# Kernel tuning notes

Hardware: AMD Instinct MI355X
Metric: run time of the kernel (lower is better)

The kernel has to match this reference:

```python
import jax, jax.numpy as jnp
import numpy as np

B, S, IN, H, C = 4, 1024, 1024, 256, 8

def setup_inputs() -> dict:
    key = jax.random.key(0)
    ks = jax.random.split(key, 9)
    scale_in = 1.0 / np.sqrt(IN)
    scale_h2 = 1.0 / np.sqrt(2 * H)
    return {
        "seq_feats": jax.random.normal(ks[0], (B, S, IN), dtype=jnp.float32),
        "U": jax.random.normal(ks[1], (H, C, H), dtype=jnp.float32) * 0.02,
        "W_weight": jax.random.uniform(ks[2], (C, 2 * H), minval=-scale_h2, maxval=scale_h2, dtype=jnp.float32),
        "W_bias": jax.random.uniform(ks[3], (C,), minval=-scale_h2, maxval=scale_h2, dtype=jnp.float32),
        "start_w": jax.random.uniform(ks[4], (H, IN), minval=-scale_in, maxval=scale_in, dtype=jnp.float32),
        "start_b": jax.random.uniform(ks[5], (H,), minval=-scale_in, maxval=scale_in, dtype=jnp.float32),
        "end_w": jax.random.uniform(ks[6], (H, IN), minval=-scale_in, maxval=scale_in, dtype=jnp.float32),
        "end_b": jax.random.uniform(ks[7], (H,), minval=-scale_in, maxval=scale_in, dtype=jnp.float32),
    }

def reference(seq_feats, U, W_weight, W_bias, start_w, start_b, end_w, end_b):
    # Hs, He: [b, s, h]
    Hs = jnp.einsum('bsi,hi->bsh', seq_feats, start_w) + start_b
    He = jnp.einsum('bsi,hi->bsh', seq_feats, end_w) + end_b
    # biaffine: [b, s, e, c]
    biaff = jnp.einsum('bsh,hcg,beg->bsec', Hs, U, He)
    # Linear over concat([Hs_repeat, He_repeat]) == split-weight broadcast sum
    Ws, We = W_weight[:, :256], W_weight[:, 256:]
    lin = (jnp.einsum('bsh,ch->bsc', Hs, Ws)[:, :, None, :]
           + jnp.einsum('beh,ch->bec', He, We)[:, None, :, :]
           + W_bias)
    return biaff + lin
```

## Files before the change

### kernel.cpp

```cpp
#include <hip/hip_runtime.h>
#include <stdint.h>


#define BDIM 256

typedef float f32x4 __attribute__((ext_vector_type(4)));
typedef __bf16 bf16x8 __attribute__((ext_vector_type(8)));
typedef unsigned int u32;
typedef unsigned short u16;
typedef const __attribute__((address_space(1))) u32* gas_ptr;
typedef __attribute__((address_space(3))) u32* las_ptr;

static __device__ __forceinline__ void load_lds16(const void* g, void* l) {
  __builtin_amdgcn_global_load_lds((gas_ptr)g, (las_ptr)l, 16, 0, 0);
}

static __device__ __forceinline__ u16 f32_to_bf16(float f) {
  union { float f; u32 u; } v; v.f = f;
  u32 r = v.u + 0x7FFFu + ((v.u >> 16) & 1u);
  return (u16)(r >> 16);
}
static __device__ __forceinline__ float bf16lo_to_f32(u32 u) {
  union { u32 u; float f; } v; v.u = u << 16;
  return v.f;
}
static __device__ __forceinline__ float bf16hi_to_f32(u32 u) {
  union { u32 u; float f; } v; v.u = u & 0xFFFF0000u;
  return v.f;
}

static __device__ __forceinline__ void stage32(u16* lds, int dst, const u16* src,
                                               int srow, int ld, int kcol, int tid) {
  const int r = tid >> 3;
  const int sl = tid & 7;
  load_lds16(src + (size_t)(srow + r) * ld + kcol + ((sl ^ (r & 7)) << 3),
             &lds[dst + tid * 8]);
}

static __device__ __forceinline__ bf16x8 rd64(const u16* lds, int base, int row, int kslot) {
  return *reinterpret_cast<const bf16x8*>(&lds[base + row * 64 + ((kslot ^ (row & 7)) << 3)]);
}

__global__ __launch_bounds__(BDIM, 4)
void gemm128_biaff(const u16* __restrict__ Tall,
                   const u16* __restrict__ Bg,
                   float* __restrict__ Out,
                   const float* __restrict__ linSall,
                   const float* __restrict__ linEall)
{
  __shared__ u16 lds[2 * 8192];

  const int tid  = threadIdx.x;
  const int lane = tid & 63;
  const int wv   = tid >> 6;
  const int wr   = wv >> 1;
  const int wc   = wv & 1;
  const int rA   = lane & 15;
  const int kq   = lane >> 4;
  const int z    = blockIdx.z;

  int id = blockIdx.y * gridDim.x + blockIdx.x;
  id = (id & 7) * 64 + (id >> 3);
  const int n0 = (id & 7) * 128;
  const int m0 = (id >> 3) * 128;

  const u16* Ag  = Tall + (size_t)z * (8192 * 256);
  const u16* Bgz = Bg   + (size_t)z * (1024 * 512);

  f32x4 acc[4][4];
#pragma unroll
  for (int i = 0; i < 4; ++i)
#pragma unroll
    for (int j = 0; j < 4; ++j) acc[i][j] = (f32x4)0.f;

#pragma unroll 1
  for (int kt = 0; kt < 256; kt += 64) {
#pragma unroll
    for (int h = 0; h < 4; ++h)
      stage32(lds, h * 2048, Ag, m0 + h * 32, 256, kt, tid);
#pragma unroll
    for (int h = 0; h < 4; ++h)
      stage32(lds, 8192 + h * 2048, Bgz, n0 + h * 32, 512, kt, tid);
    __syncthreads();

    bf16x8 aF[4][2], bF[4][2];
#pragma unroll
    for (int mi = 0; mi < 4; ++mi)
#pragma unroll
      for (int ks = 0; ks < 2; ++ks)
        aF[mi][ks] = rd64(lds, 0, wr * 64 + mi * 16 + rA, (ks << 2) | kq);
#pragma unroll
    for (int ni = 0; ni < 4; ++ni)
#pragma unroll
      for (int ks = 0; ks < 2; ++ks)
        bF[ni][ks] = rd64(lds, 8192, wc * 64 + ni * 16 + rA, (ks << 2) | kq);
#pragma unroll
    for (int mi = 0; mi < 4; ++mi)
#pragma unroll
      for (int ni = 0; ni < 4; ++ni)
#pragma unroll
        for (int ks = 0; ks < 2; ++ks)
          acc[mi][ni] = __builtin_amdgcn_mfma_f32_16x16x32_bf16(
              aF[mi][ks], bF[ni][ks], acc[mi][ni], 0, 0, 0);
    __syncthreads();
  }

  float* OutZ = Out + (size_t)z * 8388608;
  const float* lS = linSall + (size_t)z * 8192;
  const float* lE = linEall + (size_t)z * 8192;
#pragma unroll
  for (int mi = 0; mi < 4; ++mi) {
#pragma unroll
    for (int ni = 0; ni < 4; ++ni) {
      const int mBase = m0 + wr * 64 + mi * 16 + kq * 4;
      const int e = n0 + wc * 64 + ni * 16 + rA;
      const int s = mBase >> 3;
      const int c0 = mBase & 7;
      const float4 ls4 = *reinterpret_cast<const float4*>(lS + mBase);
      const float4 le4 = *reinterpret_cast<const float4*>(lE + (e << 3) + c0);
      float4 o;
      o.x = acc[mi][ni][0] + ls4.x + le4.x;
      o.y = acc[mi][ni][1] + ls4.y + le4.y;
      o.z = acc[mi][ni][2] + ls4.z + le4.z;
      o.w = acc[mi][ni][3] + ls4.w + le4.w;
      *reinterpret_cast<float4*>(OutZ + ((size_t)s << 13) + ((size_t)e << 3) + c0) = o;
    }
  }
}

template <int IM, int EPI>
__global__ __launch_bounds__(BDIM, 2)
void gemm_bt(const u16* __restrict__ Aall,
             const u16* __restrict__ Ball,
             void* __restrict__ OutAll,
             const int N, const int K, const int lda, const int ldb,
             const float* __restrict__ bias0,
             const float* __restrict__ bias1)
{
  constexpr int WM = IM * 16;
  constexpr int TM = 2 * WM;

  __shared__ u16 lsA[TM * 32];
  __shared__ u16 lsB[128 * 32];

  const int tid  = threadIdx.x;
  const int lane = tid & 63;
  const int wv   = tid >> 6;
  const int wr   = wv >> 1;
  const int wc   = wv & 1;

  const int gx = gridDim.x;
  const int nwg = gx * gridDim.y;
  int id = blockIdx.y * gx + blockIdx.x;
  {
    const int q = nwg >> 3;
    id = (id & 7) * q + (id >> 3);
  }
  const int n0 = (id % gx) * 128;
  const int m0 = (id / gx) * TM;

  const u16* A  = Aall;
  const u16* Bm = Ball;

  f32x4 acc[IM][4];
#pragma unroll
  for (int i = 0; i < IM; ++i)
#pragma unroll
    for (int j = 0; j < 4; ++j) acc[i][j] = (f32x4)0.f;

  const int rA = lane & 15;
  const int ko = (lane >> 4) * 8;

  for (int kt = 0; kt < K; kt += 32) {
    constexpr int CA = TM * 4;
#pragma unroll
    for (int it = 0; it < CA / BDIM; ++it) {
      const int chunk = it * BDIM + tid;
      const int row = chunk >> 2;
      const int ce = (chunk & 3) * 8;
      load_lds16(A + (size_t)(m0 + row) * lda + (kt + ce), &lsA[chunk * 8]);
    }
#pragma unroll
    for (int it = 0; it < 2; ++it) {
      const int chunk = it * BDIM + tid;
      const int row = chunk >> 2;
      const int ce = (chunk & 3) * 8;
      load_lds16(Bm + (size_t)(n0 + row) * ldb + (kt + ce), &lsB[chunk * 8]);
    }
    __syncthreads();

    bf16x8 aF[IM], bF[4];
#pragma unroll
    for (int i = 0; i < IM; ++i)
      aF[i] = *reinterpret_cast<const bf16x8*>(&lsA[(wr * WM + i * 16 + rA) * 32 + ko]);
#pragma unroll
    for (int j = 0; j < 4; ++j)
      bF[j] = *reinterpret_cast<const bf16x8*>(&lsB[(wc * 64 + j * 16 + rA) * 32 + ko]);
#pragma unroll
    for (int i = 0; i < IM; ++i)
#pragma unroll
      for (int j = 0; j < 4; ++j)
        acc[i][j] = __builtin_amdgcn_mfma_f32_16x16x32_bf16(aF[i], bF[j], acc[i][j], 0, 0, 0);
    __syncthreads();
  }

  const int rgr = (lane >> 4) * 4;
  u16* Out = (u16*)OutAll;
#pragma unroll
  for (int i = 0; i < IM; ++i) {
#pragma unroll
    for (int j = 0; j < 4; ++j) {
      const int mBase = m0 + wr * WM + i * 16 + rgr;
      const int n = n0 + wc * 64 + j * 16 + rA;
      float bn = 0.f;
      if constexpr (EPI == 1) bn = (n < 256) ? bias0[n] : bias1[n - 256];
#pragma unroll
      for (int r = 0; r < 4; ++r) {
        Out[(size_t)(mBase + r) * N + n] = f32_to_bf16(acc[i][j][r] + bn);
      }
    }
  }
}

__global__ __launch_bounds__(BDIM, 2)
void k2lin(const u16* __restrict__ Hboth,
           const u16* __restrict__ Utbf,
           u16* __restrict__ Tbf,
           const float* __restrict__ Ww,
           const float* __restrict__ Wb,
           float* __restrict__ linS,
           float* __restrict__ linE)
{
  const int bid = blockIdx.x;
  const int tid = threadIdx.x;

  if (bid >= 512) {
    const int idx = (bid - 512) * BDIM + tid;
    const int m = idx >> 3;
    const int c = idx & 7;
    const uint4* hs4 = reinterpret_cast<const uint4*>(Hboth + (size_t)m * 512);
    const uint4* he4 = reinterpret_cast<const uint4*>(Hboth + (size_t)m * 512 + 256);
    const float* wsp = Ww + c * 512;
    const float* wep = wsp + 256;
    float s1 = 0.f, s2 = 0.f;
#pragma unroll 4
    for (int t = 0; t < 32; ++t) {
      const uint4 a = hs4[t];
      const uint4 b = he4[t];
      const u32 aw[4] = {a.x, a.y, a.z, a.w};
      const u32 bw[4] = {b.x, b.y, b.z, b.w};
#pragma unroll
      for (int q = 0; q < 4; ++q) {
        const int h = t * 8 + q * 2;
        s1 += bf16lo_to_f32(aw[q]) * wsp[h] + bf16hi_to_f32(aw[q]) * wsp[h + 1];
        s2 += bf16lo_to_f32(bw[q]) * wep[h] + bf16hi_to_f32(bw[q]) * wep[h + 1];
      }
    }
    linS[idx] = s1;
    linE[idx] = s2 + Wb[c];
    return;
  }

  __shared__ u16 lsA[128 * 32];
  __shared__ u16 lsB[128 * 32];

  int id = bid;
  id = (id & 7) * 64 + (id >> 3);
  const int n0 = (id & 15) * 128;
  const int m0 = (id >> 4) * 128;

  const int lane = tid & 63;
  const int wv   = tid >> 6;
  const int wr   = wv >> 1;
  const int wc   = wv & 1;
  const int rA   = lane & 15;
  const int ko   = (lane >> 4) * 8;

  f32x4 acc[4][4];
#pragma unroll
  for (int i = 0; i < 4; ++i)
#pragma unroll
    for (int j = 0; j < 4; ++j) acc[i][j] = (f32x4)0.f;

  for (int kt = 0; kt < 256; kt += 32) {
#pragma unroll
    for (int it = 0; it < 2; ++it) {
      const int chunk = it * BDIM + tid;
      const int row = chunk >> 2;
      const int ce = (chunk & 3) * 8;
      load_lds16(Hboth + (size_t)(m0 + row) * 512 + (kt + ce), &lsA[chunk * 8]);
      load_lds16(Utbf + (size_t)(n0 + row) * 256 + (kt + ce), &lsB[chunk * 8]);
    }
    __syncthreads();

    bf16x8 aF[4], bF[4];
#pragma unroll
    for (int i = 0; i < 4; ++i)
      aF[i] = *reinterpret_cast<const bf16x8*>(&lsA[(wr * 64 + i * 16 + rA) * 32 + ko]);
#pragma unroll
    for (int j = 0; j < 4; ++j)
      bF[j] = *reinterpret_cast<const bf16x8*>(&lsB[(wc * 64 + j * 16 + rA) * 32 + ko]);
#pragma unroll
    for (int i = 0; i < 4; ++i)
#pragma unroll
      for (int j = 0; j < 4; ++j)
        acc[i][j] = __builtin_amdgcn_mfma_f32_16x16x32_bf16(aF[i], bF[j], acc[i][j], 0, 0, 0);
    __syncthreads();
  }

  const int rgr = (lane >> 4) * 4;
#pragma unroll
  for (int i = 0; i < 4; ++i) {
#pragma unroll
    for (int j = 0; j < 4; ++j) {
      const int mBase = m0 + wr * 64 + i * 16 + rgr;
      const int n = n0 + wc * 64 + j * 16 + rA;
#pragma unroll
      for (int r = 0; r < 4; ++r)
        Tbf[(size_t)(mBase + r) * 2048 + n] = f32_to_bf16(acc[i][j][r]);
    }
  }
}

__global__ void prep_kernel(const float* __restrict__ seq,
                            const float* __restrict__ sw,
                            const float* __restrict__ ew,
                            const float* __restrict__ U,
                            u16* __restrict__ Xbf,
                            u16* __restrict__ wbf,
                            u16* __restrict__ Ut)
{
  const int bid = blockIdx.x;
  const int tid = threadIdx.x;
  if (bid < 4096) {
    const int i = bid * 1024 + tid * 4;
    const float4 v = *reinterpret_cast<const float4*>(seq + i);
    ushort4 o;
    o.x = f32_to_bf16(v.x); o.y = f32_to_bf16(v.y);
    o.z = f32_to_bf16(v.z); o.w = f32_to_bf16(v.w);
    *reinterpret_cast<ushort4*>(Xbf + i) = o;
  } else if (bid < 4608) {
    const int i = (bid - 4096) * 1024 + tid * 4;
    const float* src = (i < 262144) ? (sw + i) : (ew + (i - 262144));
    const float4 v = *reinterpret_cast<const float4*>(src);
    ushort4 o;
    o.x = f32_to_bf16(v.x); o.y = f32_to_bf16(v.y);
    o.z = f32_to_bf16(v.z); o.w = f32_to_bf16(v.w);
    *reinterpret_cast<ushort4*>(wbf + i) = o;
  } else {
    const int i = (bid - 4608) * 1024 + tid * 4;
    const int n = i >> 8;
    const int h = i & 255;
    ushort4 o;
    o.x = f32_to_bf16(U[(size_t)(h + 0) * 2048 + n]);
    o.y = f32_to_bf16(U[(size_t)(h + 1) * 2048 + n]);
    o.z = f32_to_bf16(U[(size_t)(h + 2) * 2048 + n]);
    o.w = f32_to_bf16(U[(size_t)(h + 3) * 2048 + n]);
    *reinterpret_cast<ushort4*>(Ut + i) = o;
  }
}

extern "C" void kernel_launch(void* const* d_in, const int* in_sizes, int n_in,
                              void* d_out, int out_size, void* d_ws, size_t ws_size,
                              hipStream_t stream)
{
  const float* seq = (const float*)d_in[0];
  const float* U   = (const float*)d_in[1];
  const float* Ww  = (const float*)d_in[2];
  const float* Wb  = (const float*)d_in[3];
  const float* sw  = (const float*)d_in[4];
  const float* sb  = (const float*)d_in[5];
  const float* ew  = (const float*)d_in[6];
  const float* eb  = (const float*)d_in[7];
  float* out = (float*)d_out;

  u16* Xbf   = (u16*)d_ws;
  u16* wbf   = Xbf  + 4194304;
  u16* Utbf  = wbf  + 524288;
  u16* Hboth = Utbf + 524288;
  u16* Tbf   = Hboth + 2097152;
  float* linS = (float*)(Tbf + 8388608);
  float* linE = linS + 32768;

  prep_kernel<<<5120, BDIM, 0, stream>>>(seq, sw, ew, U, Xbf, wbf, Utbf);

  gemm_bt<2, 1><<<dim3(4, 64, 1), BDIM, 0, stream>>>(
      Xbf, wbf, Hboth, 512, 1024, 1024, 1024, sb, eb);

  k2lin<<<640, BDIM, 0, stream>>>(Hboth, Utbf, Tbf, Ww, Wb, linS, linE);

  gemm128_biaff<<<dim3(8, 64, 4), BDIM, 0, stream>>>(
      Tbf, Hboth + 256, out, linS, linE);
}
```

Before: 90.30 us.

## Fuse Hs·U projection into biaffine GEMM, keeping T tile in LDS

The T = Hs·U intermediate GEMM and the biaffine GEMM become one kernel. Each 512-thread block computes the T tile for 16 sequence positions straight into LDS as bf16, then loops over all 1024 end positions streaming He tiles against it. This removes the 16 MB Tbf round trip through global memory and one launch, and the linear-term kernel is split out on its own. In exchange the grid is only 256 blocks with 80 KB of dynamic LDS each, so occupancy drops. The U fragments are also read directly from global memory without staging.

```diff
diff --git a/kernel.cpp b/kernel.cpp
--- a/kernel.cpp
+++ b/kernel.cpp
@@ -29,101 +29,139 @@
   return v.f;
 }
 
-static __device__ __forceinline__ void stage32(u16* lds, int dst, const u16* src,
-                                               int srow, int ld, int kcol, int tid) {
-  const int r = tid >> 3;
-  const int sl = tid & 7;
-  load_lds16(src + (size_t)(srow + r) * ld + kcol + ((sl ^ (r & 7)) << 3),
-             &lds[dst + tid * 8]);
-}
-
 static __device__ __forceinline__ bf16x8 rd64(const u16* lds, int base, int row, int kslot) {
   return *reinterpret_cast<const bf16x8*>(&lds[base + row * 64 + ((kslot ^ (row & 7)) << 3)]);
 }
 
-__global__ __launch_bounds__(BDIM, 4)
-void gemm128_biaff(const u16* __restrict__ Tall,
-                   const u16* __restrict__ Bg,
-                   float* __restrict__ Out,
-                   const float* __restrict__ linSall,
-                   const float* __restrict__ linEall)
-{
-  __shared__ u16 lds[2 * 8192];
+__global__ __launch_bounds__(512, 2)
+void k23(const u16* __restrict__ Hboth,
+         const u16* __restrict__ Utbf,
+         float* __restrict__ Out,
+         const float* __restrict__ linSall,
+         const float* __restrict__ linEall)
+{
+  extern __shared__ u16 lds[];
 
   const int tid  = threadIdx.x;
   const int lane = tid & 63;
   const int wv   = tid >> 6;
-  const int wr   = wv >> 1;
-  const int wc   = wv & 1;
   const int rA   = lane & 15;
   const int kq   = lane >> 4;
-  const int z    = blockIdx.z;
-
-  int id = blockIdx.y * gridDim.x + blockIdx.x;
-  id = (id & 7) * 64 + (id >> 3);
-  const int n0 = (id & 7) * 128;
-  const int m0 = (id >> 3) * 128;
-
-  const u16* Ag  = Tall + (size_t)z * (8192 * 256);
-  const u16* Bgz = Bg   + (size_t)z * (1024 * 512);
-
-  f32x4 acc[4][4];
-#pragma unroll
-  for (int i = 0; i < 4; ++i)
-#pragma unroll
-    for (int j = 0; j < 4; ++j) acc[i][j] = (f32x4)0.f;
+
+  int id = (blockIdx.x & 7) * 32 + (blockIdx.x >> 3);
+  const int z  = id >> 6;
+  const int s0 = (id & 63) * 16;
+
+  const u16* HsZ = Hboth + ((size_t)(z * 1024 + s0)) * 512;
+  const u16* HeZ = Hboth + ((size_t)(z * 1024)) * 512 + 256;
+
+  bf16x8 bq[8];
+#pragma unroll
+  for (int ks = 0; ks < 8; ++ks)
+    bq[ks] = *reinterpret_cast<const bf16x8*>(HsZ + (size_t)rA * 512 + ks * 32 + kq * 8);
+
+  f32x4 p[16];
+#pragma unroll
+  for (int t = 0; t < 16; ++t) p[t] = (f32x4)0.f;
+
+  const u16* UtW = Utbf + ((size_t)(wv * 256 + rA)) * 256 + kq * 8;
+#pragma unroll
+  for (int ks = 0; ks < 8; ++ks) {
+#pragma unroll
+    for (int t = 0; t < 16; ++t) {
+      const bf16x8 a = *reinterpret_cast<const bf16x8*>(UtW + t * 16 * 256 + ks * 32);
+      p[t] = __builtin_amdgcn_mfma_f32_16x16x32_bf16(a, bq[ks], p[t], 0, 0, 0);
+    }
+  }
+
+  {
+    const int m = rA * 8 + wv;
+    const int mbase = m * 64;
+#pragma unroll
+    for (int t = 0; t < 16; ++t) {
+      ushort4 w4;
+      w4.x = f32_to_bf16(p[t][0]);
+      w4.y = f32_to_bf16(p[t][1]);
+      w4.z = f32_to_bf16(p[t][2]);
+      w4.w = f32_to_bf16(p[t][3]);
+      const int kslot = (t & 3) * 2 + (kq >> 1);
+      const int addr = (t >> 2) * 8192 + mbase + ((kslot ^ wv) << 3) + (kq & 1) * 4;
+      *reinterpret_cast<ushort4*>(&lds[addr]) = w4;
+    }
+  }
+  __syncthreads();
+
+  const int wr = wv >> 2;
+  const int wc = wv & 3;
+
+  float* OutZ = Out + (size_t)z * 8388608;
+  const float* lS = linSall + ((size_t)(z * 1024 + s0)) * 8;
+  const float* lE = linEall + (size_t)z * 8192;
+
+  float4 ls4[4];
+#pragma unroll
+  for (int mi = 0; mi < 4; ++mi)
+    ls4[mi] = *reinterpret_cast<const float4*>(lS + wr * 64 + mi * 16 + kq * 4);
 
 #pragma unroll 1
-  for (int kt = 0; kt < 256; kt += 64) {
-#pragma unroll
-    for (int h = 0; h < 4; ++h)
-      stage32(lds, h * 2048, Ag, m0 + h * 32, 256, kt, tid);
-#pragma unroll
-    for (int h = 0; h < 4; ++h)
-      stage32(lds, 8192 + h * 2048, Bgz, n0 + h * 32, 512, kt, tid);
-    __syncthreads();
-
-    bf16x8 aF[4][2], bF[4][2];
-#pragma unroll
-    for (int mi = 0; mi < 4; ++mi)
-#pragma unroll
-      for (int ks = 0; ks < 2; ++ks)
-        aF[mi][ks] = rd64(lds, 0, wr * 64 + mi * 16 + rA, (ks << 2) | kq);
-#pragma unroll
-    for (int ni = 0; ni < 4; ++ni)
-#pragma unroll
-      for (int ks = 0; ks < 2; ++ks)
-        bF[ni][ks] = rd64(lds, 8192, wc * 64 + ni * 16 + rA, (ks << 2) | kq);
-#pragma unroll
-    for (int mi = 0; mi < 4; ++mi)
-#pragma unroll
-      for (int ni = 0; ni < 4; ++ni)
+  for (int nt = 0; nt < 8; ++nt) {
+    const int e0 = nt * 128;
+    f32x4 acc[4][2];
+#pragma unroll
+    for (int i = 0; i < 4; ++i)
+#pragma unroll
+      for (int j = 0; j < 2; ++j) acc[i][j] = (f32x4)0.f;
+
+#pragma unroll 1
+    for (int kt = 0; kt < 4; ++kt) {
+#pragma unroll
+      for (int hh = 0; hh < 2; ++hh) {
+        const int idx = hh * 512 + tid;
+        const int r = idx >> 3;
+        const int sl = idx & 7;
+        load_lds16(HeZ + (size_t)(e0 + r) * 512 + kt * 64 + ((sl ^ (r & 7)) << 3),
+                   &lds[32768 + idx * 8]);
+      }
+      __syncthreads();
+
+      bf16x8 aF[4][2], bF[2][2];
+#pragma unroll
+      for (int mi = 0; mi < 4; ++mi)
 #pragma unroll
         for (int ks = 0; ks < 2; ++ks)
-          acc[mi][ni] = __builtin_amdgcn_mfma_f32_16x16x32_bf16(
-              aF[mi][ks], bF[ni][ks], acc[mi][ni], 0, 0, 0);
-    __syncthreads();
-  }
-
-  float* OutZ = Out + (size_t)z * 8388608;
-  const float* lS = linSall + (size_t)z * 8192;
-  const float* lE = linEall + (size_t)z * 8192;
-#pragma unroll
-  for (int mi = 0; mi < 4; ++mi) {
-#pragma unroll
-    for (int ni = 0; ni < 4; ++ni) {
-      const int mBase = m0 + wr * 64 + mi * 16 + kq * 4;
-      const int e = n0 + wc * 64 + ni * 16 + rA;
+          aF[mi][ks] = rd64(lds, kt * 8192, wr * 64 + mi * 16 + rA, (ks << 2) | kq);
+#pragma unroll
+      for (int ni = 0; ni < 2; ++ni)
+#pragma unroll
+        for (int ks = 0; ks < 2; ++ks)
+          bF[ni][ks] = rd64(lds, 32768, wc * 32 + ni * 16 + rA, (ks << 2) | kq);
+#pragma unroll
+      for (int mi = 0; mi < 4; ++mi)
+#pragma unroll
+        for (int ni = 0; ni < 2; ++ni)
+#pragma unroll
+          for (int ks = 0; ks < 2; ++ks)
+            acc[mi][ni] = __builtin_amdgcn_mfma_f32_16x16x32_bf16(
+                aF[mi][ks], bF[ni][ks], acc[mi][ni], 0, 0, 0);
+      __syncthreads();
+    }
+
+#pragma unroll
+    for (int mi = 0; mi < 4; ++mi) {
+      const int mBase = wr * 64 + mi * 16 + kq * 4;
       const int s = mBase >> 3;
       const int c0 = mBase & 7;
-      const float4 ls4 = *reinterpret_cast<const float4*>(lS + mBase);
-      const float4 le4 = *reinterpret_cast<const float4*>(lE + (e << 3) + c0);
-      float4 o;
-      o.x = acc[mi][ni][0] + ls4.x + le4.x;
-      o.y = acc[mi][ni][1] + ls4.y + le4.y;
-      o.z = acc[mi][ni][2] + ls4.z + le4.z;
-      o.w = acc[mi][ni][3] + ls4.w + le4.w;
-      *reinterpret_cast<float4*>(OutZ + ((size_t)s << 13) + ((size_t)e << 3) + c0) = o;
+#pragma unroll
+      for (int ni = 0; ni < 2; ++ni) {
+        const int e = e0 + wc * 32 + ni * 16 + rA;
+        const float4 le4 = *reinterpret_cast<const float4*>(lE + e * 8 + c0);
+        float4 o;
+        o.x = acc[mi][ni][0] + ls4[mi].x + le4.x;
+        o.y = acc[mi][ni][1] + ls4[mi].y + le4.y;
+        o.z = acc[mi][ni][2] + ls4[mi].z + le4.z;
+        o.w = acc[mi][ni][3] + ls4[mi].w + le4.w;
+        *reinterpret_cast<float4*>(OutZ + (((size_t)(s0 + s)) << 13) + ((size_t)e << 3) + c0) = o;
+      }
     }
   }
 }
@@ -222,104 +260,36 @@
   }
 }
 
-__global__ __launch_bounds__(BDIM, 2)
-void k2lin(const u16* __restrict__ Hboth,
-           const u16* __restrict__ Utbf,
-           u16* __restrict__ Tbf,
-           const float* __restrict__ Ww,
-           const float* __restrict__ Wb,
-           float* __restrict__ linS,
-           float* __restrict__ linE)
-{
-  const int bid = blockIdx.x;
-  const int tid = threadIdx.x;
-
-  if (bid >= 512) {
-    const int idx = (bid - 512) * BDIM + tid;
-    const int m = idx >> 3;
-    const int c = idx & 7;
-    const uint4* hs4 = reinterpret_cast<const uint4*>(Hboth + (size_t)m * 512);
-    const uint4* he4 = reinterpret_cast<const uint4*>(Hboth + (size_t)m * 512 + 256);
-    const float* wsp = Ww + c * 512;
-    const float* wep = wsp + 256;
-    float s1 = 0.f, s2 = 0.f;
+__global__ __launch_bounds__(BDIM)
+void lin_kernel(const u16* __restrict__ Hboth,
+                const float* __restrict__ Ww,
+                const float* __restrict__ Wb,
+                float* __restrict__ linS,
+                float* __restrict__ linE)
+{
+  const int idx = blockIdx.x * BDIM + threadIdx.x;
+  const int m = idx >> 3;
+  const int c = idx & 7;
+  const uint4* hs4 = reinterpret_cast<const uint4*>(Hboth + (size_t)m * 512);
+  const uint4* he4 = reinterpret_cast<const uint4*>(Hboth + (size_t)m * 512 + 256);
+  const float* wsp = Ww + c * 512;
+  const float* wep = wsp + 256;
+  float s1 = 0.f, s2 = 0.f;
 #pragma unroll 4
-    for (int t = 0; t < 32; ++t) {
-      const uint4 a = hs4[t];
-      const uint4 b = he4[t];
-      const u32 aw[4] = {a.x, a.y, a.z, a.w};
-      const u32 bw[4] = {b.x, b.y, b.z, b.w};
-#pragma unroll
-      for (int q = 0; q < 4; ++q) {
-        const int h = t * 8 + q * 2;
-        s1 += bf16lo_to_f32(aw[q]) * wsp[h] + bf16hi_to_f32(aw[q]) * wsp[h + 1];
-        s2 += bf16lo_to_f32(bw[q]) * wep[h] + bf16hi_to_f32(bw[q]) * wep[h + 1];
-      }
-    }
-    linS[idx] = s1;
-    linE[idx] = s2 + Wb[c];
-    return;
-  }
-
-  __shared__ u16 lsA[128 * 32];
-  __shared__ u16 lsB[128 * 32];
-
-  int id = bid;
-  id = (id & 7) * 64 + (id >> 3);
-  const int n0 = (id & 15) * 128;
-  const int m0 = (id >> 4) * 128;
-
-  const int lane = tid & 63;
-  const int wv   = tid >> 6;
-  const int wr   = wv >> 1;
-  const int wc   = wv & 1;
-  const int rA   = lane & 15;
-  const int ko   = (lane >> 4) * 8;
-
-  f32x4 acc[4][4];
-#pragma unroll
-  for (int i = 0; i < 4; ++i)
-#pragma unroll
-    for (int j = 0; j < 4; ++j) acc[i][j] = (f32x4)0.f;
-
-  for (int kt = 0; kt < 256; kt += 32) {
-#pragma unroll
-    for (int it = 0; it < 2; ++it) {
-      const int chunk = it * BDIM + tid;
-      const int row = chunk >> 2;
-      const int ce = (chunk & 3) * 8;
-      load_lds16(Hboth + (size_t)(m0 + row) * 512 + (kt + ce), &lsA[chunk * 8]);
-      load_lds16(Utbf + (size_t)(n0 + row) * 256 + (kt + ce), &lsB[chunk * 8]);
-    }
-    __syncthreads();
-
-    bf16x8 aF[4], bF[4];
-#pragma unroll
-    for (int i = 0; i < 4; ++i)
-      aF[i] = *reinterpret_cast<const bf16x8*>(&lsA[(wr * 64 + i * 16 + rA) * 32 + ko]);
-#pragma unroll
-    for (int j = 0; j < 4; ++j)
-      bF[j] = *reinterpret_cast<const bf16x8*>(&lsB[(wc * 64 + j * 16 + rA) * 32 + ko]);
-#pragma unroll
-    for (int i = 0; i < 4; ++i)
-#pragma unroll
-      for (int j = 0; j < 4; ++j)
-        acc[i][j] = __builtin_amdgcn_mfma_f32_16x16x32_bf16(aF[i], bF[j], acc[i][j], 0, 0, 0);
-    __syncthreads();
-  }
-
-  const int rgr = (lane >> 4) * 4;
-#pragma unroll
-  for (int i = 0; i < 4; ++i) {
-#pragma unroll
-    for (int j = 0; j < 4; ++j) {
-      const int mBase = m0 + wr * 64 + i * 16 + rgr;
-      const int n = n0 + wc * 64 + j * 16 + rA;
-#pragma unroll
-      for (int r = 0; r < 4; ++r)
-        Tbf[(size_t)(mBase + r) * 2048 + n] = f32_to_bf16(acc[i][j][r]);
-    }
-  }
+  for (int t = 0; t < 32; ++t) {
+    const uint4 a = hs4[t];
+    const uint4 b = he4[t];
+    const u32 aw[4] = {a.x, a.y, a.z, a.w};
+    const u32 bw[4] = {b.x, b.y, b.z, b.w};
+#pragma unroll
+    for (int q = 0; q < 4; ++q) {
+      const int h = t * 8 + q * 2;
+      s1 += bf16lo_to_f32(aw[q]) * wsp[h] + bf16hi_to_f32(aw[q]) * wsp[h + 1];
+      s2 += bf16lo_to_f32(bw[q]) * wep[h] + bf16hi_to_f32(bw[q]) * wep[h + 1];
+    }
+  }
+  linS[idx] = s1;
+  linE[idx] = s2 + Wb[c];
 }
 
 __global__ void prep_kernel(const float* __restrict__ seq,
@@ -378,8 +348,7 @@
   u16* wbf   = Xbf  + 4194304;
   u16* Utbf  = wbf  + 524288;
   u16* Hboth = Utbf + 524288;
-  u16* Tbf   = Hboth + 2097152;
-  float* linS = (float*)(Tbf + 8388608);
+  float* linS = (float*)(Hboth + 2097152);
   float* linE = linS + 32768;
 
   prep_kernel<<<5120, BDIM, 0, stream>>>(seq, sw, ew, U, Xbf, wbf, Utbf);
@@ -387,8 +356,9 @@
   gemm_bt<2, 1><<<dim3(4, 64, 1), BDIM, 0, stream>>>(
       Xbf, wbf, Hboth, 512, 1024, 1024, 1024, sb, eb);
 
-  k2lin<<<640, BDIM, 0, stream>>>(Hboth, Utbf, Tbf, Ww, Wb, linS, linE);
-
-  gemm128_biaff<<<dim3(8, 64, 4), BDIM, 0, stream>>>(
-      Tbf, Hboth + 256, out, linS, linE);
-}
+  lin_kernel<<<128, BDIM, 0, stream>>>(Hboth, Ww, Wb, linS, linE);
+
+  hipFuncSetAttribute(reinterpret_cast<const void*>(&k23),
+                      hipFuncAttributeMaxDynamicSharedMemorySize, 81920);
+  k23<<<256, 512, 81920, stream>>>(Hboth, Utbf, out, linS, linE);
+}
```

Measured after the change: 123.7 us. 37.0% more time.

## Replace projection GEMM with 64x64-tile swizzled-LDS kernel using K=64 steps

Applied to the files above, without the earlier changes.

Replaces the generic gemm_bt used for the Hs/He projection with a dedicated kernel that uses 64x64 output tiles, a 512-block grid, and K steps of 64 staged through an XOR-swizzled LDS layout. The smaller tiles double the block count, which should fill more CUs, and the swizzle should cut LDS bank conflicts. The cost is lower per-block data reuse and more global traffic per FLOP. The launch also allows higher occupancy via launch bounds of 4.

```diff
diff --git a/kernel.cpp b/kernel.cpp
--- a/kernel.cpp
+++ b/kernel.cpp
@@ -39,6 +39,78 @@
 
 static __device__ __forceinline__ bf16x8 rd64(const u16* lds, int base, int row, int kslot) {
   return *reinterpret_cast<const bf16x8*>(&lds[base + row * 64 + ((kslot ^ (row & 7)) << 3)]);
+}
+
+__global__ __launch_bounds__(BDIM, 4)
+void k1(const u16* __restrict__ Xbf,
+        const u16* __restrict__ wbf,
+        u16* __restrict__ Hboth,
+        const float* __restrict__ sb,
+        const float* __restrict__ eb)
+{
+  __shared__ u16 lds[2 * 4096];
+
+  const int tid  = threadIdx.x;
+  const int lane = tid & 63;
+  const int wv   = tid >> 6;
+  const int wr   = wv >> 1;
+  const int wq   = wv & 1;
+  const int rA   = lane & 15;
+  const int kq   = lane >> 4;
+
+  int id = blockIdx.y * gridDim.x + blockIdx.x;
+  id = (id & 7) * 64 + (id >> 3);
+  const int n0 = (id & 7) * 64;
+  const int m0 = (id >> 3) * 64;
+
+  f32x4 acc[2][2];
+#pragma unroll
+  for (int i = 0; i < 2; ++i)
+#pragma unroll
+    for (int j = 0; j < 2; ++j) acc[i][j] = (f32x4)0.f;
+
+#pragma unroll 1
+  for (int kt = 0; kt < 1024; kt += 64) {
+    stage32(lds, 0,        Xbf, m0,      1024, kt, tid);
+    stage32(lds, 2048,     Xbf, m0 + 32, 1024, kt, tid);
+    stage32(lds, 4096,     wbf, n0,      1024, kt, tid);
+    stage32(lds, 4096+2048,wbf, n0 + 32, 1024, kt, tid);
+    __syncthreads();
+
+    bf16x8 aF[2][2], bF[2][2];
+#pragma unroll
+    for (int mi = 0; mi < 2; ++mi)
+#pragma unroll
+      for (int ks = 0; ks < 2; ++ks)
+        aF[mi][ks] = rd64(lds, 0, wr * 32 + mi * 16 + rA, (ks << 2) | kq);
+#pragma unroll
+    for (int ni = 0; ni < 2; ++ni)
+#pragma unroll
+      for (int ks = 0; ks < 2; ++ks)
+        bF[ni][ks] = rd64(lds, 4096, wq * 32 + ni * 16 + rA, (ks << 2) | kq);
+#pragma unroll
+    for (int mi = 0; mi < 2; ++mi)
+#pragma unroll
+      for (int ni = 0; ni < 2; ++ni)
+#pragma unroll
+        for (int ks = 0; ks < 2; ++ks)
+          acc[mi][ni] = __builtin_amdgcn_mfma_f32_16x16x32_bf16(
+              aF[mi][ks], bF[ni][ks], acc[mi][ni], 0, 0, 0);
+    __syncthreads();
+  }
+
+#pragma unroll
+  for (int mi = 0; mi < 2; ++mi) {
+#pragma unroll
+    for (int ni = 0; ni < 2; ++ni) {
+      const int n = n0 + wq * 32 + ni * 16 + rA;
+      const float bn = (n < 256) ? sb[n] : eb[n - 256];
+      const int mr = m0 + wr * 32 + mi * 16 + kq * 4;
+#pragma unroll
+      for (int r = 0; r < 4; ++r)
+        Hboth[(size_t)(mr + r) * 512 + n] = f32_to_bf16(acc[mi][ni][r] + bn);
+    }
+  }
 }
 
 __global__ __launch_bounds__(BDIM, 4)
@@ -124,100 +196,6 @@
       o.z = acc[mi][ni][2] + ls4.z + le4.z;
       o.w = acc[mi][ni][3] + ls4.w + le4.w;
       *reinterpret_cast<float4*>(OutZ + ((size_t)s << 13) + ((size_t)e << 3) + c0) = o;
-    }
-  }
-}
-
-template <int IM, int EPI>
-__global__ __launch_bounds__(BDIM, 2)
-void gemm_bt(const u16* __restrict__ Aall,
-             const u16* __restrict__ Ball,
-             void* __restrict__ OutAll,
-             const int N, const int K, const int lda, const int ldb,
-             const float* __restrict__ bias0,
-             const float* __restrict__ bias1)
-{
-  constexpr int WM = IM * 16;
-  constexpr int TM = 2 * WM;
-
-  __shared__ u16 lsA[TM * 32];
-  __shared__ u16 lsB[128 * 32];
-
-  const int tid  = threadIdx.x;
-  const int lane = tid & 63;
-  const int wv   = tid >> 6;
-  const int wr   = wv >> 1;
-  const int wc   = wv & 1;
-
-  const int gx = gridDim.x;
-  const int nwg = gx * gridDim.y;
-  int id = blockIdx.y * gx + blockIdx.x;
-  {
-    const int q = nwg >> 3;
-    id = (id & 7) * q + (id >> 3);
-  }
-  const int n0 = (id % gx) * 128;
-  const int m0 = (id / gx) * TM;
-
-  const u16* A  = Aall;
-  const u16* Bm = Ball;
-
-  f32x4 acc[IM][4];
-#pragma unroll
-  for (int i = 0; i < IM; ++i)
-#pragma unroll
-    for (int j = 0; j < 4; ++j) acc[i][j] = (f32x4)0.f;
-
-  const int rA = lane & 15;
-  const int ko = (lane >> 4) * 8;
-
-  for (int kt = 0; kt < K; kt += 32) {
-    constexpr int CA = TM * 4;
-#pragma unroll
-    for (int it = 0; it < CA / BDIM; ++it) {
-      const int chunk = it * BDIM + tid;
-      const int row = chunk >> 2;
-      const int ce = (chunk & 3) * 8;
-      load_lds16(A + (size_t)(m0 + row) * lda + (kt + ce), &lsA[chunk * 8]);
-    }
-#pragma unroll
-    for (int it = 0; it < 2; ++it) {
-      const int chunk = it * BDIM + tid;
-      const int row = chunk >> 2;
-      const int ce = (chunk & 3) * 8;
-      load_lds16(Bm + (size_t)(n0 + row) * ldb + (kt + ce), &lsB[chunk * 8]);
-    }
-    __syncthreads();
-
-    bf16x8 aF[IM], bF[4];
-#pragma unroll
-    for (int i = 0; i < IM; ++i)
-      aF[i] = *reinterpret_cast<const bf16x8*>(&lsA[(wr * WM + i * 16 + rA) * 32 + ko]);
-#pragma unroll
-    for (int j = 0; j < 4; ++j)
-      bF[j] = *reinterpret_cast<const bf16x8*>(&lsB[(wc * 64 + j * 16 + rA) * 32 + ko]);
-#pragma unroll
-    for (int i = 0; i < IM; ++i)
-#pragma unroll
-      for (int j = 0; j < 4; ++j)
-        acc[i][j] = __builtin_amdgcn_mfma_f32_16x16x32_bf16(aF[i], bF[j], acc[i][j], 0, 0, 0);
-    __syncthreads();
-  }
-
-  const int rgr = (lane >> 4) * 4;
-  u16* Out = (u16*)OutAll;
-#pragma unroll
-  for (int i = 0; i < IM; ++i) {
-#pragma unroll
-    for (int j = 0; j < 4; ++j) {
-      const int mBase = m0 + wr * WM + i * 16 + rgr;
-      const int n = n0 + wc * 64 + j * 16 + rA;
-      float bn = 0.f;
-      if constexpr (EPI == 1) bn = (n < 256) ? bias0[n] : bias1[n - 256];
-#pragma unroll
-      for (int r = 0; r < 4; ++r) {
-        Out[(size_t)(mBase + r) * N + n] = f32_to_bf16(acc[i][j][r] + bn);
-      }
     }
   }
 }
@@ -384,8 +362,7 @@
 
   prep_kernel<<<5120, BDIM, 0, stream>>>(seq, sw, ew, U, Xbf, wbf, Utbf);
 
-  gemm_bt<2, 1><<<dim3(4, 64, 1), BDIM, 0, stream>>>(
-      Xbf, wbf, Hboth, 512, 1024, 1024, 1024, sb, eb);
+  k1<<<dim3(8, 64, 1), BDIM, 0, stream>>>(Xbf, wbf, Hboth, sb, eb);
 
   k2lin<<<640, BDIM, 0, stream>>>(Hboth, Utbf, Tbf, Ww, Wb, linS, linE);
 
```

New measurement: 85.19 us. -5.7%, faster.
